# Performance work log

Hardware: AMD Instinct MI355X
Metric: run time of the kernel (lower is better)

## Reference

```python
import jax, jax.numpy as jnp
import numpy as np

K = 1024
HEADS = 16


def setup_inputs() -> dict:
    key = jax.random.key(0)
    ks = jax.random.split(key, 6)
    x = jax.random.normal(ks[0], (2, 2048, K), dtype=jnp.float32)
    sc = 1.0 / np.sqrt(K)
    Wq = jax.random.normal(ks[1], (K, K), dtype=jnp.float32) * sc
    Wk = jax.random.normal(ks[2], (K, K), dtype=jnp.float32) * sc
    Wv = jax.random.normal(ks[3], (K, K), dtype=jnp.float32) * sc
    Wu = jax.random.normal(ks[4], (K, K), dtype=jnp.float32) * sc
    bu = jax.random.normal(ks[5], (K,), dtype=jnp.float32) * 0.01
    return {"x": x, "Wq": Wq, "Wk": Wk, "Wv": Wv, "Wu": Wu, "bu": bu}


def reference(x, Wq, Wk, Wv, Wu, bu):
    b, t, k = x.shape
    h = HEADS
    s = k // h
    # torch Linear: y = x @ W.T
    q = (x @ Wq.T).reshape(b, t, h, s)
    kk = (x @ Wk.T).reshape(b, t, h, s)
    v = (x @ Wv.T).reshape(b, t, h, s)
    # NOTE: original scales by sqrt(k) (full model dim), not sqrt(head dim)
    dot = jnp.einsum('bqhs,bkhs->bhqk', q, kk) / jnp.sqrt(jnp.float32(k))
    attn = jax.nn.softmax(dot, axis=-1)
    out = jnp.einsum('bhqk,bkhs->bqhs', attn, v).reshape(b, t, k)
    return out @ Wu.T + bu
```

## Files before the change

kernel.cpp:

```cpp
#include <hip/hip_runtime.h>
#include <hip/hip_bf16.h>


typedef __bf16 bf16x8 __attribute__((ext_vector_type(8)));
typedef float f32x4 __attribute__((ext_vector_type(4)));
typedef float f32x16 __attribute__((ext_vector_type(16)));
typedef unsigned int u32x4 __attribute__((ext_vector_type(4)));

static __device__ __forceinline__ unsigned short f2bf(float f) {
  union { float f; unsigned u; } a; a.f = f;
  unsigned r = a.u + 0x7fff + ((a.u >> 16) & 1);
  return (unsigned short)(r >> 16);
}

static __device__ __forceinline__ unsigned cvt_pk_bf16(float lo, float hi) {
  unsigned r;
  asm("v_cvt_pk_bf16_f32 %0, %1, %2" : "=v"(r) : "v"(lo), "v"(hi));
  return r;
}

static __device__ __forceinline__ float fexp2(float x) {
#if __has_builtin(__builtin_amdgcn_exp2f)
  return __builtin_amdgcn_exp2f(x);
#else
  float r; asm("v_exp_f32 %0, %1\n\ts_nop 0" : "=v"(r) : "v"(x)); return r;
#endif
}

static __device__ __forceinline__ void wv8() { asm volatile("s_waitcnt vmcnt(8)" ::: "memory"); }
static __device__ __forceinline__ void wv4() { asm volatile("s_waitcnt vmcnt(4)" ::: "memory"); }
static __device__ __forceinline__ void wv0() { asm volatile("s_waitcnt vmcnt(0)" ::: "memory"); }

static __device__ __forceinline__ void swap32(unsigned a, unsigned b,
                                              unsigned& x, unsigned& y, int hi) {
#if __has_builtin(__builtin_amdgcn_permlane32_swap)
  typedef unsigned u32x2 __attribute__((ext_vector_type(2)));
  u32x2 r = __builtin_amdgcn_permlane32_swap(a, b, false, false);
  x = r.x; y = r.y;
#else
  unsigned pa = (unsigned)__shfl_xor((int)a, 32, 64);
  unsigned pb = (unsigned)__shfl_xor((int)b, 32, 64);
  x = hi ? pb : a;
  y = hi ? b : pa;
#endif
}

static __device__ __forceinline__ void gload_lds16(const unsigned short* g, unsigned short* l) {
  __builtin_amdgcn_global_load_lds((const __attribute__((address_space(1))) void*)g,
                                   (__attribute__((address_space(3))) void*)l, 16, 0, 0);
}

static __device__ __forceinline__ float tsum16(const f32x16& v) {
  float a0 = v[0]+v[1], a1 = v[2]+v[3], a2 = v[4]+v[5], a3 = v[6]+v[7];
  float a4 = v[8]+v[9], a5 = v[10]+v[11], a6 = v[12]+v[13], a7 = v[14]+v[15];
  float b0 = a0+a1, b1 = a2+a3, b2 = a4+a5, b3 = a6+a7;
  return (b0+b1) + (b2+b3);
}

__global__ __launch_bounds__(256)
void cast_all(const float* __restrict__ x, const float* __restrict__ wq,
              const float* __restrict__ wk, const float* __restrict__ wv,
              const float* __restrict__ wu,
              unsigned short* __restrict__ xb, unsigned short* __restrict__ wqb,
              unsigned short* __restrict__ wkb, unsigned short* __restrict__ wvb,
              unsigned short* __restrict__ wub)
{
  int bid = blockIdx.x;
  const float* src; unsigned short* dst; int blk;
  if (bid < 4096)      { src = x;  dst = xb;  blk = bid; }
  else if (bid < 5120) { src = wq; dst = wqb; blk = bid - 4096; }
  else if (bid < 6144) { src = wk; dst = wkb; blk = bid - 5120; }
  else if (bid < 7168) { src = wv; dst = wvb; blk = bid - 6144; }
  else                 { src = wu; dst = wub; blk = bid - 7168; }
  int idx = blk * 1024 + threadIdx.x * 4;
  float4 v = *(const float4*)&src[idx];
  ushort4 o;
  o.x = f2bf(v.x); o.y = f2bf(v.y); o.z = f2bf(v.z); o.w = f2bf(v.w);
  *(ushort4*)&dst[idx] = o;
}

__global__ __launch_bounds__(512, 2)
void gemm_qkv(const unsigned short* __restrict__ A,
              const unsigned short* __restrict__ Bq,
              const unsigned short* __restrict__ Bk,
              const unsigned short* __restrict__ Bv,
              unsigned short* __restrict__ Qo,
              unsigned short* __restrict__ Ko,
              unsigned short* __restrict__ Vo)
{
  const int Ksz = 1024;
  __shared__ __align__(16) unsigned short As[2][128 * 64];
  __shared__ __align__(16) unsigned short Bs[2][128 * 64];
  const int z = blockIdx.z;
  const unsigned short* B = (z == 0) ? Bq : (z == 1) ? Bk : Bv;
  const int tid  = threadIdx.x;
  const int lane = tid & 63;
  const int wid  = tid >> 6;
  const int wr   = wid >> 2, wc = wid & 3;
  const int g    = lane >> 4, r = lane & 15;
  const int bm   = blockIdx.x * 128, bn = blockIdx.y * 128;

  f32x4 acc[4][2] = {};

  const int srow   = lane >> 3;
  const int schunk = (lane & 7) ^ srow;
  const unsigned short* Ag0 = &A[(size_t)(bm + wid*16 +     srow) * Ksz + schunk*8];
  const unsigned short* Ag1 = &A[(size_t)(bm + wid*16 + 8 + srow) * Ksz + schunk*8];
  const unsigned short* Bg0 = &B[(size_t)(bn + wid*16 +     srow) * Ksz + schunk*8];
  const unsigned short* Bg1 = &B[(size_t)(bn + wid*16 + 8 + srow) * Ksz + schunk*8];

  auto stage_step = [&](int kof, int b) {
    gload_lds16(Ag0 + kof, &As[b][(wid*16    ) * 64]);
    gload_lds16(Ag1 + kof, &As[b][(wid*16 + 8) * 64]);
    gload_lds16(Bg0 + kof, &Bs[b][(wid*16    ) * 64]);
    gload_lds16(Bg1 + kof, &Bs[b][(wid*16 + 8) * 64]);
  };

  stage_step(0,  0);
  stage_step(64, 1);
  wv4();
  __builtin_amdgcn_s_barrier();

#pragma unroll 1
  for (int ks = 0; ks < 16; ++ks) {
    const int buf = ks & 1;
#pragma unroll
    for (int kk = 0; kk < 2; ++kk) {
      bf16x8 af[4], bfr[2];
#pragma unroll
      for (int mi = 0; mi < 4; ++mi) {
        int row = wr*64 + mi*16 + r;
        int c = (g + kk*4) ^ (row & 7);
        af[mi] = *(const bf16x8*)&As[buf][row*64 + c*8];
      }
#pragma unroll
      for (int ni = 0; ni < 2; ++ni) {
        int row = wc*32 + ni*16 + r;
        int c = (g + kk*4) ^ (row & 7);
        bfr[ni] = *(const bf16x8*)&Bs[buf][row*64 + c*8];
      }
#pragma unroll
      for (int mi = 0; mi < 4; ++mi)
#pragma unroll
        for (int ni = 0; ni < 2; ++ni)
          acc[mi][ni] = __builtin_amdgcn_mfma_f32_16x16x32_bf16(af[mi], bfr[ni], acc[mi][ni], 0, 0, 0);
    }
    if (ks == 15) break;
    __builtin_amdgcn_s_barrier();
    if (ks + 2 < 16) { stage_step((ks + 2) * 64, buf); wv4(); }
    else             { wv0(); }
    __builtin_amdgcn_s_barrier();
  }

  const float scale = (z == 0) ? (0.03125f * 1.4426950408889634f) : 1.0f;
#pragma unroll
  for (int mi = 0; mi < 4; ++mi)
#pragma unroll
    for (int ni = 0; ni < 2; ++ni) {
      if (z == 2) {
        int m0 = bm + wr*64 + mi*16 + g*4;
        int n  = bn + wc*32 + ni*16 + r;
        int b = m0 >> 11, t0 = m0 & 2047;
        int h = n >> 6,  s = n & 63;
        ushort4 o;
        o.x = f2bf(acc[mi][ni][0]); o.y = f2bf(acc[mi][ni][1]);
        o.z = f2bf(acc[mi][ni][2]); o.w = f2bf(acc[mi][ni][3]);
        *(ushort4*)&Vo[((size_t)((b*16 + h)*64 + s)) * 2048 + t0] = o;
      } else {
        unsigned short* dst = (z == 0) ? Qo : Ko;
#pragma unroll
        for (int q = 0; q < 4; ++q) {
          int m = bm + wr*64 + mi*16 + g*4 + q;
          int n = bn + wc*32 + ni*16 + r;
          int b = m >> 11, t = m & 2047;
          int h = n >> 6,  s = n & 63;
          dst[((size_t)((b*16 + h)*2048 + t)) * 64 + s] = f2bf(acc[mi][ni][q] * scale);
        }
      }
    }
}

__global__ __launch_bounds__(512, 2)
void gemm_final(const unsigned short* __restrict__ A,
                const unsigned short* __restrict__ B,
                float* __restrict__ Cf,
                const float* __restrict__ bias)
{
  const int Ksz = 1024, N = 1024;
  __shared__ __align__(16) unsigned short As[2][128 * 64];
  __shared__ __align__(16) unsigned short Bs[2][128 * 64];
  const int tid  = threadIdx.x;
  const int lane = tid & 63;
  const int wid  = tid >> 6;
  const int wr   = wid >> 2, wc = wid & 3;
  const int g    = lane >> 4, r = lane & 15;
  const int bm   = blockIdx.x * 128, bn = blockIdx.y * 128;

  f32x4 acc[4][2] = {};

  const int srow   = lane >> 3;
  const int schunk = (lane & 7) ^ srow;
  const unsigned short* Ag0 = &A[(size_t)(bm + wid*16 +     srow) * Ksz + schunk*8];
  const unsigned short* Ag1 = &A[(size_t)(bm + wid*16 + 8 + srow) * Ksz + schunk*8];
  const unsigned short* Bg0 = &B[(size_t)(bn + wid*16 +     srow) * Ksz + schunk*8];
  const unsigned short* Bg1 = &B[(size_t)(bn + wid*16 + 8 + srow) * Ksz + schunk*8];

  auto stage_step = [&](int kof, int b) {
    gload_lds16(Ag0 + kof, &As[b][(wid*16    ) * 64]);
    gload_lds16(Ag1 + kof, &As[b][(wid*16 + 8) * 64]);
    gload_lds16(Bg0 + kof, &Bs[b][(wid*16    ) * 64]);
    gload_lds16(Bg1 + kof, &Bs[b][(wid*16 + 8) * 64]);
  };

  stage_step(0,  0);
  stage_step(64, 1);
  wv4();
  __builtin_amdgcn_s_barrier();

#pragma unroll 1
  for (int ks = 0; ks < 16; ++ks) {
    const int buf = ks & 1;
#pragma unroll
    for (int kk = 0; kk < 2; ++kk) {
      bf16x8 af[4], bfr[2];
#pragma unroll
      for (int mi = 0; mi < 4; ++mi) {
        int row = wr*64 + mi*16 + r;
        int c = (g + kk*4) ^ (row & 7);
        af[mi] = *(const bf16x8*)&As[buf][row*64 + c*8];
      }
#pragma unroll
      for (int ni = 0; ni < 2; ++ni) {
        int row = wc*32 + ni*16 + r;
        int c = (g + kk*4) ^ (row & 7);
        bfr[ni] = *(const bf16x8*)&Bs[buf][row*64 + c*8];
      }
#pragma unroll
      for (int mi = 0; mi < 4; ++mi)
#pragma unroll
        for (int ni = 0; ni < 2; ++ni)
          acc[mi][ni] = __builtin_amdgcn_mfma_f32_16x16x32_bf16(af[mi], bfr[ni], acc[mi][ni], 0, 0, 0);
    }
    if (ks == 15) break;
    __builtin_amdgcn_s_barrier();
    if (ks + 2 < 16) { stage_step((ks + 2) * 64, buf); wv4(); }
    else             { wv0(); }
    __builtin_amdgcn_s_barrier();
  }

#pragma unroll
  for (int mi = 0; mi < 4; ++mi)
#pragma unroll
    for (int ni = 0; ni < 2; ++ni)
#pragma unroll
      for (int q = 0; q < 4; ++q) {
        int m = bm + wr*64 + mi*16 + g*4 + q;
        int n = bn + wc*32 + ni*16 + r;
        Cf[(size_t)m * N + n] = acc[mi][ni][q] + bias[n];
      }
}

__global__ __launch_bounds__(256)
void attn_kernel(const unsigned short* __restrict__ Qg,
                 const unsigned short* __restrict__ Kg,
                 const unsigned short* __restrict__ Vtg,
                 unsigned short* __restrict__ Og)
{
  const int T = 2048;
  __shared__ __align__(16) unsigned short sK[2][128 * 64];
  __shared__ __align__(16) unsigned short sV[2][64 * 128];

  const int tid = threadIdx.x, lane = tid & 63, wid = tid >> 6;
  const int q32 = lane & 31;
  const int kh  = lane >> 5;

  int bid  = blockIdx.x + 16 * blockIdx.y;
  int nb   = (bid & 7) * 64 + (bid >> 3);
  int bh   = nb >> 4;
  int qblk = nb & 15;
  int qbase = qblk * 128 + wid * 32;

  const size_t base = (size_t)bh * T * 64;
  const unsigned short* Qh = Qg + base;
  const unsigned short* Kh = Kg + base;
  const unsigned short* Vh = Vtg + base;

  const int krow_l  = lane >> 3;
  const int kchunk  = (lane & 7) ^ (krow_l & 7);
  const int vrow_l  = lane >> 4;
  const int vchunkp = lane & 15;

  auto stage_tile = [&](int kvb, int b) {
#pragma unroll
    for (int rr = 0; rr < 4; ++rr) {
      int kr = rr*32 + wid*8;
      gload_lds16(Kh + (size_t)(kvb + kr + krow_l)*64 + kchunk*8, &sK[b][kr*64]);
      int vr = rr*16 + wid*4;
      int vrow = vr + vrow_l;
      gload_lds16(Vh + (size_t)vrow*T + kvb + ((vchunkp ^ (vrow & 7))*8), &sV[b][vr*128]);
    }
  };

  bf16x8 qf[4];
#pragma unroll
  for (int s = 0; s < 4; ++s)
    qf[s] = *(const bf16x8*)&Qh[(size_t)(qbase + q32)*64 + s*16 + kh*8];

  f32x16 oacc[2] = {};
  float l_own = 0.f;

  stage_tile(0,   0);
  stage_tile(128, 1);
  wv8();
  __builtin_amdgcn_s_barrier();

#pragma unroll 1
  for (int t = 0; t < 16; ++t) {
    const int buf = t & 1;

#pragma unroll
    for (int st = 0; st < 4; ++st) {
      f32x16 a = {};
      const int kvr = st*32 + q32;
#pragma unroll
      for (int s = 0; s < 4; ++s) {
        const int c = (s*2 + kh) ^ (kvr & 7);
        bf16x8 kf = *(const bf16x8*)&sK[buf][kvr*64 + c*8];
        a = __builtin_amdgcn_mfma_f32_32x32x16_bf16(kf, qf[s], a, 0, 0, 0);
      }
#pragma unroll
      for (int rr = 0; rr < 16; ++rr)
        a[rr] = fexp2(a[rr]);
      l_own += tsum16(a);

      unsigned U[8];
#pragma unroll
      for (int i = 0; i < 8; ++i)
        U[i] = cvt_pk_bf16(a[2*i], a[2*i + 1]);
      unsigned w[8];
      swap32(U[0], U[2], w[0], w[2], kh);
      swap32(U[1], U[3], w[1], w[3], kh);
      swap32(U[4], U[6], w[4], w[6], kh);
      swap32(U[5], U[7], w[5], w[7], kh);
#pragma unroll
      for (int c = 0; c < 2; ++c) {
        u32x4 pw = { w[c*4 + 0], w[c*4 + 1], w[c*4 + 2], w[c*4 + 3] };
        bf16x8 pf = __builtin_bit_cast(bf16x8, pw);
#pragma unroll
        for (int mt = 0; mt < 2; ++mt) {
          const int sr = mt*32 + q32;
          const int cc = (st*4 + c*2 + kh) ^ (sr & 7);
          bf16x8 vfr = *(const bf16x8*)&sV[buf][sr*128 + cc*8];
          oacc[mt] = __builtin_amdgcn_mfma_f32_32x32x16_bf16(vfr, pf, oacc[mt], 0, 0, 0);
        }
      }
    }

    if (t == 15) break;
    __builtin_amdgcn_s_barrier();
    if (t + 2 < 16) { stage_tile((t + 2) * 128, buf); wv8(); }
    else            { wv0(); }
    __builtin_amdgcn_s_barrier();
  }

  const float l = l_own + __shfl_xor(l_own, 32, 64);
  const int h = bh & 15, b = bh >> 4;
  const float inv = 1.0f / l;
  const int tq = qbase + q32;
#pragma unroll
  for (int mt = 0; mt < 2; ++mt)
#pragma unroll
    for (int rg = 0; rg < 4; ++rg) {
      ushort4 o;
      o.x = f2bf(oacc[mt][rg*4 + 0] * inv);
      o.y = f2bf(oacc[mt][rg*4 + 1] * inv);
      o.z = f2bf(oacc[mt][rg*4 + 2] * inv);
      o.w = f2bf(oacc[mt][rg*4 + 3] * inv);
      int sd = mt*32 + rg*8 + kh*4;
      *(ushort4*)&Og[((size_t)(b*2048 + tq))*1024 + h*64 + sd] = o;
    }
}

extern "C" void kernel_launch(void* const* d_in, const int* in_sizes, int n_in,
                              void* d_out, int out_size, void* d_ws, size_t ws_size,
                              hipStream_t stream) {
  const float* x  = (const float*)d_in[0];
  const float* Wq = (const float*)d_in[1];
  const float* Wk = (const float*)d_in[2];
  const float* Wv = (const float*)d_in[3];
  const float* Wu = (const float*)d_in[4];
  const float* bu = (const float*)d_in[5];
  float* out = (float*)d_out;

  char* ws = (char*)d_ws;
  unsigned short* xb  = (unsigned short*)(ws);
  unsigned short* Wqb = (unsigned short*)(ws + (size_t)( 8<<20));
  unsigned short* Wkb = (unsigned short*)(ws + (size_t)(10<<20));
  unsigned short* Wvb = (unsigned short*)(ws + (size_t)(12<<20));
  unsigned short* Wub = (unsigned short*)(ws + (size_t)(14<<20));
  unsigned short* Qg  = (unsigned short*)(ws + (size_t)(16<<20));
  unsigned short* Kg  = (unsigned short*)(ws + (size_t)(24<<20));
  unsigned short* Vtg = (unsigned short*)(ws + (size_t)(32<<20));
  unsigned short* Ab  = xb;

  cast_all<<<dim3(8192), 256, 0, stream>>>(x, Wq, Wk, Wv, Wu, xb, Wqb, Wkb, Wvb, Wub);

  gemm_qkv<<<dim3(32, 8, 3), 512, 0, stream>>>(xb, Wqb, Wkb, Wvb, Qg, Kg, Vtg);

  attn_kernel<<<dim3(16, 32), 256, 0, stream>>>(Qg, Kg, Vtg, Ab);

  gemm_final<<<dim3(32, 8), 512, 0, stream>>>(Ab, Wub, out, bu);
}
```

Measured before the change: 107.6 us.

## Rework attention kernel to 16x16 MFMA with 8 waves and LDS P staging

The attention kernel moves from 4 waves with 32x32x16 MFMAs to 8 waves per block, each owning 16 query rows and using 16x16x32 MFMAs. The exp'd scores are now converted to bf16 and routed through a small per-wave LDS buffer, replacing the permlane32 swap, to form the P operand for the PV MFMA. Staging is split across the 8 waves, with 2 loads per wave per tile. The aim is more waves in flight and lower register pressure, at the cost of extra LDS writes and reads per score tile and smaller MFMA shapes. The softmax has no max subtraction, unchanged from before.

```diff
diff --git a/kernel.cpp b/kernel.cpp
--- a/kernel.cpp
+++ b/kernel.cpp
@@ -4,7 +4,6 @@
 
 typedef __bf16 bf16x8 __attribute__((ext_vector_type(8)));
 typedef float f32x4 __attribute__((ext_vector_type(4)));
-typedef float f32x16 __attribute__((ext_vector_type(16)));
 typedef unsigned int u32x4 __attribute__((ext_vector_type(4)));
 
 static __device__ __forceinline__ unsigned short f2bf(float f) {
@@ -27,34 +26,12 @@
 #endif
 }
 
-static __device__ __forceinline__ void wv8() { asm volatile("s_waitcnt vmcnt(8)" ::: "memory"); }
 static __device__ __forceinline__ void wv4() { asm volatile("s_waitcnt vmcnt(4)" ::: "memory"); }
 static __device__ __forceinline__ void wv0() { asm volatile("s_waitcnt vmcnt(0)" ::: "memory"); }
-
-static __device__ __forceinline__ void swap32(unsigned a, unsigned b,
-                                              unsigned& x, unsigned& y, int hi) {
-#if __has_builtin(__builtin_amdgcn_permlane32_swap)
-  typedef unsigned u32x2 __attribute__((ext_vector_type(2)));
-  u32x2 r = __builtin_amdgcn_permlane32_swap(a, b, false, false);
-  x = r.x; y = r.y;
-#else
-  unsigned pa = (unsigned)__shfl_xor((int)a, 32, 64);
-  unsigned pb = (unsigned)__shfl_xor((int)b, 32, 64);
-  x = hi ? pb : a;
-  y = hi ? b : pa;
-#endif
-}
 
 static __device__ __forceinline__ void gload_lds16(const unsigned short* g, unsigned short* l) {
   __builtin_amdgcn_global_load_lds((const __attribute__((address_space(1))) void*)g,
                                    (__attribute__((address_space(3))) void*)l, 16, 0, 0);
-}
-
-static __device__ __forceinline__ float tsum16(const f32x16& v) {
-  float a0 = v[0]+v[1], a1 = v[2]+v[3], a2 = v[4]+v[5], a3 = v[6]+v[7];
-  float a4 = v[8]+v[9], a5 = v[10]+v[11], a6 = v[12]+v[13], a7 = v[14]+v[15];
-  float b0 = a0+a1, b1 = a2+a3, b2 = a4+a5, b3 = a6+a7;
-  return (b0+b1) + (b2+b3);
 }
 
 __global__ __launch_bounds__(256)
@@ -260,7 +237,7 @@
       }
 }
 
-__global__ __launch_bounds__(256)
+__global__ __launch_bounds__(512)
 void attn_kernel(const unsigned short* __restrict__ Qg,
                  const unsigned short* __restrict__ Kg,
                  const unsigned short* __restrict__ Vtg,
@@ -269,116 +246,109 @@
   const int T = 2048;
   __shared__ __align__(16) unsigned short sK[2][128 * 64];
   __shared__ __align__(16) unsigned short sV[2][64 * 128];
+  __shared__ __align__(16) unsigned short Pl[8 * 16 * 40];
 
   const int tid = threadIdx.x, lane = tid & 63, wid = tid >> 6;
-  const int q32 = lane & 31;
-  const int kh  = lane >> 5;
+  const int g = lane >> 4, r = lane & 15;
 
   int bid  = blockIdx.x + 16 * blockIdx.y;
   int nb   = (bid & 7) * 64 + (bid >> 3);
   int bh   = nb >> 4;
   int qblk = nb & 15;
-  int qbase = qblk * 128 + wid * 32;
+  const int qbase = qblk * 128 + wid * 16;
 
   const size_t base = (size_t)bh * T * 64;
   const unsigned short* Qh = Qg + base;
   const unsigned short* Kh = Kg + base;
   const unsigned short* Vh = Vtg + base;
 
-  const int krow_l  = lane >> 3;
-  const int kchunk  = (lane & 7) ^ (krow_l & 7);
-  const int vrow_l  = lane >> 4;
-  const int vchunkp = lane & 15;
-
+  const int krl = lane >> 3;
+  const int kch = (lane & 7) ^ (krl & 7);
+  const int vrl = lane >> 4;
   auto stage_tile = [&](int kvb, int b) {
 #pragma unroll
-    for (int rr = 0; rr < 4; ++rr) {
-      int kr = rr*32 + wid*8;
-      gload_lds16(Kh + (size_t)(kvb + kr + krow_l)*64 + kchunk*8, &sK[b][kr*64]);
-      int vr = rr*16 + wid*4;
-      int vrow = vr + vrow_l;
-      gload_lds16(Vh + (size_t)vrow*T + kvb + ((vchunkp ^ (vrow & 7))*8), &sV[b][vr*128]);
+    for (int i = 0; i < 2; ++i) {
+      int krow = i*64 + wid*8;
+      gload_lds16(Kh + (size_t)(kvb + krow + krl)*64 + kch*8,
+                  &sK[b][krow * 64]);
+      int vrow = i*32 + wid*4;
+      int vr_f = vrow + vrl;
+      gload_lds16(Vh + (size_t)vr_f*T + kvb + (((lane & 15) ^ (vr_f & 7)))*8,
+                  &sV[b][vrow * 128]);
     }
   };
 
-  bf16x8 qf[4];
-#pragma unroll
-  for (int s = 0; s < 4; ++s)
-    qf[s] = *(const bf16x8*)&Qh[(size_t)(qbase + q32)*64 + s*16 + kh*8];
-
-  f32x16 oacc[2] = {};
+  bf16x8 qf[2];
+#pragma unroll
+  for (int ks = 0; ks < 2; ++ks)
+    qf[ks] = *(const bf16x8*)&Qh[(size_t)(qbase + r)*64 + ks*32 + g*8];
+
+  unsigned short* Plw = &Pl[wid * 640];
+
+  f32x4 oacc[4] = {};
   float l_own = 0.f;
 
   stage_tile(0,   0);
   stage_tile(128, 1);
-  wv8();
+  wv4();
   __builtin_amdgcn_s_barrier();
 
 #pragma unroll 1
   for (int t = 0; t < 16; ++t) {
-    const int buf = t & 1;
-
-#pragma unroll
-    for (int st = 0; st < 4; ++st) {
-      f32x16 a = {};
-      const int kvr = st*32 + q32;
-#pragma unroll
-      for (int s = 0; s < 4; ++s) {
-        const int c = (s*2 + kh) ^ (kvr & 7);
-        bf16x8 kf = *(const bf16x8*)&sK[buf][kvr*64 + c*8];
-        a = __builtin_amdgcn_mfma_f32_32x32x16_bf16(kf, qf[s], a, 0, 0, 0);
-      }
-#pragma unroll
-      for (int rr = 0; rr < 16; ++rr)
-        a[rr] = fexp2(a[rr]);
-      l_own += tsum16(a);
-
-      unsigned U[8];
-#pragma unroll
-      for (int i = 0; i < 8; ++i)
-        U[i] = cvt_pk_bf16(a[2*i], a[2*i + 1]);
-      unsigned w[8];
-      swap32(U[0], U[2], w[0], w[2], kh);
-      swap32(U[1], U[3], w[1], w[3], kh);
-      swap32(U[4], U[6], w[4], w[6], kh);
-      swap32(U[5], U[7], w[5], w[7], kh);
-#pragma unroll
-      for (int c = 0; c < 2; ++c) {
-        u32x4 pw = { w[c*4 + 0], w[c*4 + 1], w[c*4 + 2], w[c*4 + 3] };
-        bf16x8 pf = __builtin_bit_cast(bf16x8, pw);
-#pragma unroll
-        for (int mt = 0; mt < 2; ++mt) {
-          const int sr = mt*32 + q32;
-          const int cc = (st*4 + c*2 + kh) ^ (sr & 7);
-          bf16x8 vfr = *(const bf16x8*)&sV[buf][sr*128 + cc*8];
-          oacc[mt] = __builtin_amdgcn_mfma_f32_32x32x16_bf16(vfr, pf, oacc[mt], 0, 0, 0);
+    const unsigned short* sKb = sK[t & 1];
+    const unsigned short* sVb = sV[t & 1];
+
+#pragma unroll
+    for (int cc = 0; cc < 4; ++cc) {
+#pragma unroll
+      for (int stl = 0; stl < 2; ++stl) {
+        const int st = cc*2 + stl;
+        f32x4 a = {};
+#pragma unroll
+        for (int ks = 0; ks < 2; ++ks) {
+          const int c = (ks*4 + g) ^ (r & 7);
+          bf16x8 kf = *(const bf16x8*)&sKb[(st*16 + r)*64 + c*8];
+          a = __builtin_amdgcn_mfma_f32_16x16x32_bf16(kf, qf[ks], a, 0, 0, 0);
         }
+        a[0] = fexp2(a[0]); a[1] = fexp2(a[1]);
+        a[2] = fexp2(a[2]); a[3] = fexp2(a[3]);
+        l_own += (a[0] + a[1]) + (a[2] + a[3]);
+        uint2 w;
+        w.x = cvt_pk_bf16(a[0], a[1]);
+        w.y = cvt_pk_bf16(a[2], a[3]);
+        *(uint2*)&Plw[r*40 + (stl*4 + g)*4] = w;
+      }
+      bf16x8 pf = *(const bf16x8*)&Plw[r*40 + 8*g];
+#pragma unroll
+      for (int sv = 0; sv < 4; ++sv) {
+        const int c = (cc*4 + g) ^ (r & 7);
+        bf16x8 vfr = *(const bf16x8*)&sVb[(sv*16 + r)*128 + c*8];
+        oacc[sv] = __builtin_amdgcn_mfma_f32_16x16x32_bf16(vfr, pf, oacc[sv], 0, 0, 0);
       }
     }
 
     if (t == 15) break;
     __builtin_amdgcn_s_barrier();
-    if (t + 2 < 16) { stage_tile((t + 2) * 128, buf); wv8(); }
+    if (t + 2 < 16) { stage_tile((t + 2) * 128, t & 1); wv4(); }
     else            { wv0(); }
     __builtin_amdgcn_s_barrier();
   }
 
-  const float l = l_own + __shfl_xor(l_own, 32, 64);
+  l_own += __shfl_xor(l_own, 16, 64);
+  l_own += __shfl_xor(l_own, 32, 64);
+  const float inv = 1.0f / l_own;
   const int h = bh & 15, b = bh >> 4;
-  const float inv = 1.0f / l;
-  const int tq = qbase + q32;
-#pragma unroll
-  for (int mt = 0; mt < 2; ++mt)
-#pragma unroll
-    for (int rg = 0; rg < 4; ++rg) {
-      ushort4 o;
-      o.x = f2bf(oacc[mt][rg*4 + 0] * inv);
-      o.y = f2bf(oacc[mt][rg*4 + 1] * inv);
-      o.z = f2bf(oacc[mt][rg*4 + 2] * inv);
-      o.w = f2bf(oacc[mt][rg*4 + 3] * inv);
-      int sd = mt*32 + rg*8 + kh*4;
-      *(ushort4*)&Og[((size_t)(b*2048 + tq))*1024 + h*64 + sd] = o;
-    }
+  const int tq = qbase + r;
+#pragma unroll
+  for (int sv = 0; sv < 4; ++sv) {
+    ushort4 o;
+    o.x = f2bf(oacc[sv][0] * inv);
+    o.y = f2bf(oacc[sv][1] * inv);
+    o.z = f2bf(oacc[sv][2] * inv);
+    o.w = f2bf(oacc[sv][3] * inv);
+    int sd = sv*16 + g*4;
+    *(ushort4*)&Og[((size_t)(b*2048 + tq))*1024 + h*64 + sd] = o;
+  }
 }
 
 extern "C" void kernel_launch(void* const* d_in, const int* in_sizes, int n_in,
@@ -407,7 +377,7 @@
 
   gemm_qkv<<<dim3(32, 8, 3), 512, 0, stream>>>(xb, Wqb, Wkb, Wvb, Qg, Kg, Vtg);
 
-  attn_kernel<<<dim3(16, 32), 256, 0, stream>>>(Qg, Kg, Vtg, Ab);
+  attn_kernel<<<dim3(16, 32), 512, 0, stream>>>(Qg, Kg, Vtg, Ab);
 
   gemm_final<<<dim3(32, 8), 512, 0, stream>>>(Ab, Wub, out, bu);
 }
```

Result: slower. 112.7 us (+4.7%).
